# Performance work log

Measured on AMD Instinct MI355X. Metric: run time of the kernel, lower is better.

Reference implementation:

```python
import jax, jax.numpy as jnp
import numpy as np

N_NODES = 100000


def _gcn_conv(x, row, col, W, b, num_nodes):
    """PyG GCNConv: symmetric normalization with self-loops, then linear.
    row/col already include self-loops. x: [N, d_in], W: [d_in, d_out]."""
    xw = x @ W  # [N, d_out]
    ones = jnp.ones(row.shape[0], dtype=x.dtype)
    deg = jax.ops.segment_sum(ones, col, num_segments=num_nodes)  # in-degree incl self-loop
    deg_inv_sqrt = jnp.where(deg > 0, jax.lax.rsqrt(jnp.maximum(deg, 1e-12)), 0.0)
    norm = deg_inv_sqrt[row] * deg_inv_sqrt[col]  # [E]
    msgs = xw[row] * norm[:, None]  # gather + scale, [E, d_out]
    out = jax.ops.segment_sum(msgs, col, num_segments=num_nodes)  # scatter-add
    return out + b


def _add_self_loops(edge_index, num_nodes):
    loop = jnp.arange(num_nodes, dtype=edge_index.dtype)
    row = jnp.concatenate([edge_index[0], loop])
    col = jnp.concatenate([edge_index[1], loop])
    return row, col


def setup_inputs() -> dict:
    key = jax.random.key(0)
    k_x, k_e, k_w1, k_b1, k_w2, k_b2 = jax.random.split(key, 6)
    in_dim, hidden_dim, out_dim = 64, 64, 32
    n_edges = 1600000
    x = jax.random.normal(k_x, (N_NODES, in_dim), dtype=jnp.float32)
    edge_index = jax.random.randint(k_e, (2, n_edges), 0, N_NODES, dtype=jnp.int64)
    # Glorot init like PyG's GCNConv linear weights
    s1 = float(np.sqrt(6.0 / (in_dim + hidden_dim)))
    s2 = float(np.sqrt(6.0 / (hidden_dim + out_dim)))
    W1 = jax.random.uniform(k_w1, (in_dim, hidden_dim), minval=-s1, maxval=s1, dtype=jnp.float32)
    b1 = jnp.zeros((hidden_dim,), dtype=jnp.float32)
    W2 = jax.random.uniform(k_w2, (hidden_dim, out_dim), minval=-s2, maxval=s2, dtype=jnp.float32)
    b2 = jnp.zeros((out_dim,), dtype=jnp.float32)
    return {"x": x, "edge_index": edge_index, "W1": W1, "b1": b1, "W2": W2, "b2": b2}


def reference(x, edge_index, W1, b1, W2, b2):
    row, col = _add_self_loops(edge_index, N_NODES)
    h = jax.nn.relu(_gcn_conv(x, row, col, W1, b1, N_NODES))
    out = _gcn_conv(h, row, col, W2, b2, N_NODES)
    return out
```

## Files before the change

kernel.cpp:

```cpp
#include <hip/hip_runtime.h>

#define NN 100000
#define FB_SH 10
#define FB_N  1024
#define NFB   98
#define NBLK  256
#define BH_TOT (NFB * NBLK)

static __device__ __forceinline__ unsigned short f2bf(float f) {
    unsigned u = __float_as_uint(f);
    u += 0x7fffu + ((u >> 16) & 1u);
    return (unsigned short)(u >> 16);
}
static __device__ __forceinline__ float bf2f(unsigned short h) {
    return __uint_as_float(((unsigned)h) << 16);
}


__global__ __launch_bounds__(256) void k_hist1(const int* __restrict__ coli,
                                               int* __restrict__ bhist, int E, int chunk) {
    __shared__ int h[NFB];
    for (int i = threadIdx.x; i < NFB; i += 256) h[i] = 0;
    __syncthreads();
    int bk = blockIdx.x;
    int beg = bk * chunk, end = min(E, beg + chunk);
    for (int e = beg + threadIdx.x; e < end; e += 256)
        atomicAdd(&h[coli[e] >> FB_SH], 1);
    __syncthreads();
    for (int i = threadIdx.x; i < NFB; i += 256)
        bhist[i * NBLK + bk] = h[i];
}

__global__ __launch_bounds__(1024) void k_scanA(int* __restrict__ a,
                                                int* __restrict__ blksum, int n) {
    __shared__ int sh[1024];
    int i = blockIdx.x * 1024 + threadIdx.x;
    int v = (i < n) ? a[i] : 0;
    sh[threadIdx.x] = v;
    __syncthreads();
    #pragma unroll
    for (int d = 1; d < 1024; d <<= 1) {
        int t = (threadIdx.x >= d) ? sh[threadIdx.x - d] : 0;
        __syncthreads();
        sh[threadIdx.x] += t;
        __syncthreads();
    }
    if (i < n) a[i] = sh[threadIdx.x] - v;
    if (threadIdx.x == 1023) blksum[blockIdx.x] = sh[1023];
}

__global__ void k_scanB(int* __restrict__ blksum, int nb, int* __restrict__ off, int E) {
    if (threadIdx.x == 0 && blockIdx.x == 0) {
        int s = 0;
        for (int b = 0; b < nb; ++b) { int t = blksum[b]; blksum[b] = s; s += t; }
        off[NN] = E;
    }
}

__global__ __launch_bounds__(256) void k_scanC(int* __restrict__ a,
                                               const int* __restrict__ blksum, int n) {
    int i = blockIdx.x * 256 + threadIdx.x;
    if (i < n) a[i] += blksum[i >> 10];
}

__global__ __launch_bounds__(256) void k_bin2(
    const int* __restrict__ rowi, const int* __restrict__ coli,
    const int* __restrict__ bbase, unsigned int* __restrict__ cbin, int E, int chunk)
{
    __shared__ int cur[NFB];
    int bk = blockIdx.x;
    for (int i = threadIdx.x; i < NFB; i += 256) cur[i] = bbase[i * NBLK + bk];
    __syncthreads();
    int beg = bk * chunk, end = min(E, beg + chunk);
    for (int e = beg + threadIdx.x; e < end; e += 256) {
        int col = coli[e];
        int row = rowi[e];
        int b = col >> FB_SH;
        unsigned int val = ((unsigned int)row << FB_SH) | (unsigned int)(col & (FB_N - 1));
        int pos = atomicAdd(&cur[b], 1);
        cbin[pos] = val;
    }
}

__global__ __launch_bounds__(1024) void k_csr(
    const unsigned int* __restrict__ cbin, const int* __restrict__ bbase,
    int* __restrict__ off, float* __restrict__ dinv,
    int* __restrict__ srcs, int n, int E)
{
    __shared__ int hist[FB_N];
    __shared__ int wsum[16];
    int b = blockIdx.x;
    int beg = bbase[b * NBLK];
    int end = (b + 1 < NFB) ? bbase[(b + 1) * NBLK] : E;
    int tid = threadIdx.x;
    hist[tid] = 0;
    __syncthreads();
    for (int e = beg + tid; e < end; e += 1024)
        atomicAdd(&hist[cbin[e] & (FB_N - 1)], 1);
    __syncthreads();
    int v = hist[tid];
    int lane = tid & 63;
    int wid  = tid >> 6;
    int incl = v;
    #pragma unroll
    for (int d = 1; d < 64; d <<= 1) {
        int t = __shfl_up(incl, d, 64);
        if (lane >= d) incl += t;
    }
    if (lane == 63) wsum[wid] = incl;
    __syncthreads();
    if (wid == 0) {
        int ws = (lane < 16) ? wsum[lane] : 0;
        int wincl = ws;
        #pragma unroll
        for (int d = 1; d < 16; d <<= 1) {
            int t = __shfl_up(wincl, d, 64);
            if (lane >= d) wincl += t;
        }
        if (lane < 16) wsum[lane] = wincl - ws;
    }
    __syncthreads();
    int excl = wsum[wid] + incl - v;
    int node = (b << FB_SH) + tid;
    if (node < n) {
        off[node]  = beg + excl;
        dinv[node] = rsqrtf((float)(v + 1));
    }
    __syncthreads();
    hist[tid] = excl;
    __syncthreads();
    for (int e = beg + tid; e < end; e += 1024) {
        unsigned int pv = cbin[e];
        int cl  = (int)(pv & (FB_N - 1));
        int row = (int)(pv >> FB_SH);
        int p = atomicAdd(&hist[cl], 1);
        srcs[beg + p] = row;
    }
}

template<int DOUT>
__global__ __launch_bounds__(256) void k_gemm_scale(
    const float* __restrict__ X, const float* __restrict__ W,
    const float* __restrict__ dinv, unsigned short* __restrict__ Ybf, int n)
{
    constexpr int TPR = DOUT / 4;
    constexpr int R   = 256 / TPR;
    __shared__ float sW[64 * DOUT];
    __shared__ float sX[R * 64];

    for (int i = threadIdx.x; i < 64 * DOUT; i += 256) sW[i] = W[i];
    int r0 = blockIdx.x * R;
    for (int i = threadIdx.x; i < R * 64; i += 256) {
        int r = r0 + (i >> 6);
        sX[i] = (r < n) ? X[(size_t)r * 64 + (i & 63)] : 0.0f;
    }
    __syncthreads();

    int lr  = threadIdx.x / TPR;
    int c4  = (threadIdx.x % TPR) * 4;
    int row = r0 + lr;
    const float* xr = &sX[lr * 64];
    float4 acc = make_float4(0.f, 0.f, 0.f, 0.f);
    #pragma unroll
    for (int k = 0; k < 64; ++k) {
        float xv = xr[k];
        const float* wr = &sW[k * DOUT + c4];
        acc.x = fmaf(xv, wr[0], acc.x);
        acc.y = fmaf(xv, wr[1], acc.y);
        acc.z = fmaf(xv, wr[2], acc.z);
        acc.w = fmaf(xv, wr[3], acc.w);
    }
    if (row < n) {
        float s = dinv[row];
        ushort4 o;
        o.x = f2bf(acc.x * s);
        o.y = f2bf(acc.y * s);
        o.z = f2bf(acc.z * s);
        o.w = f2bf(acc.w * s);
        *(ushort4*)&Ybf[(size_t)row * DOUT + c4] = o;
    }
}

template<bool RELU>
__global__ __launch_bounds__(256) void k_agg64(
    const unsigned short* __restrict__ Ybf, const int* __restrict__ off,
    const int* __restrict__ srcs, const float* __restrict__ dinv,
    const float* __restrict__ bias, float* __restrict__ O, int n)
{
    int node = blockIdx.x * 4 + (threadIdx.x >> 6);
    if (node >= n) return;
    int c = threadIdx.x & 63;
    int j = off[node], end = off[node + 1];
    float s0 = bf2f(Ybf[(size_t)node * 64 + c]);
    float s1 = 0.f, s2 = 0.f, s3 = 0.f, s4 = 0.f, s5 = 0.f, s6 = 0.f, s7 = 0.f;
    for (; j + 8 <= end; j += 8) {
        int i0 = srcs[j],     i1 = srcs[j + 1], i2 = srcs[j + 2], i3 = srcs[j + 3];
        int i4 = srcs[j + 4], i5 = srcs[j + 5], i6 = srcs[j + 6], i7 = srcs[j + 7];
        unsigned short r0 = Ybf[(size_t)i0 * 64 + c];
        unsigned short r1 = Ybf[(size_t)i1 * 64 + c];
        unsigned short r2 = Ybf[(size_t)i2 * 64 + c];
        unsigned short r3 = Ybf[(size_t)i3 * 64 + c];
        unsigned short r4 = Ybf[(size_t)i4 * 64 + c];
        unsigned short r5 = Ybf[(size_t)i5 * 64 + c];
        unsigned short r6 = Ybf[(size_t)i6 * 64 + c];
        unsigned short r7 = Ybf[(size_t)i7 * 64 + c];
        s0 += bf2f(r0); s1 += bf2f(r1); s2 += bf2f(r2); s3 += bf2f(r3);
        s4 += bf2f(r4); s5 += bf2f(r5); s6 += bf2f(r6); s7 += bf2f(r7);
    }
    for (; j < end; ++j) s0 += bf2f(Ybf[(size_t)srcs[j] * 64 + c]);
    float s = ((s0 + s1) + (s2 + s3)) + ((s4 + s5) + (s6 + s7));
    float o = fmaf(dinv[node], s, bias[c]);
    if (RELU) o = fmaxf(o, 0.f);
    O[(size_t)node * 64 + c] = o;
}

template<bool RELU>
__global__ __launch_bounds__(256) void k_agg32(
    const unsigned short* __restrict__ Ybf, const int* __restrict__ off,
    const int* __restrict__ srcs, const float* __restrict__ dinv,
    const float* __restrict__ bias, float* __restrict__ O, int n)
{
    int node = blockIdx.x * 8 + (threadIdx.x >> 5);
    if (node >= n) return;
    int c = threadIdx.x & 31;
    int j = off[node], end = off[node + 1];
    float s0 = bf2f(Ybf[(size_t)node * 32 + c]);
    float s1 = 0.f, s2 = 0.f, s3 = 0.f, s4 = 0.f, s5 = 0.f, s6 = 0.f, s7 = 0.f;
    for (; j + 8 <= end; j += 8) {
        int i0 = srcs[j],     i1 = srcs[j + 1], i2 = srcs[j + 2], i3 = srcs[j + 3];
        int i4 = srcs[j + 4], i5 = srcs[j + 5], i6 = srcs[j + 6], i7 = srcs[j + 7];
        unsigned short r0 = Ybf[(size_t)i0 * 32 + c];
        unsigned short r1 = Ybf[(size_t)i1 * 32 + c];
        unsigned short r2 = Ybf[(size_t)i2 * 32 + c];
        unsigned short r3 = Ybf[(size_t)i3 * 32 + c];
        unsigned short r4 = Ybf[(size_t)i4 * 32 + c];
        unsigned short r5 = Ybf[(size_t)i5 * 32 + c];
        unsigned short r6 = Ybf[(size_t)i6 * 32 + c];
        unsigned short r7 = Ybf[(size_t)i7 * 32 + c];
        s0 += bf2f(r0); s1 += bf2f(r1); s2 += bf2f(r2); s3 += bf2f(r3);
        s4 += bf2f(r4); s5 += bf2f(r5); s6 += bf2f(r6); s7 += bf2f(r7);
    }
    for (; j < end; ++j) s0 += bf2f(Ybf[(size_t)srcs[j] * 32 + c]);
    float s = ((s0 + s1) + (s2 + s3)) + ((s4 + s5) + (s6 + s7));
    float o = fmaf(dinv[node], s, bias[c]);
    if (RELU) o = fmaxf(o, 0.f);
    O[(size_t)node * 32 + c] = o;
}

extern "C" void kernel_launch(void* const* d_in, const int* in_sizes, int n_in,
                              void* d_out, int out_size, void* d_ws, size_t ws_size,
                              hipStream_t stream) {
    const float* x  = (const float*)d_in[0];
    const int*   ei = (const int*)d_in[1];
    const float* W1 = (const float*)d_in[2];
    const float* b1 = (const float*)d_in[3];
    const float* W2 = (const float*)d_in[4];
    const float* b2 = (const float*)d_in[5];
    float* out = (float*)d_out;

    const int n = NN;
    const int E = in_sizes[1] / 2;
    const int* rowi = ei;
    const int* coli = ei + E;
    const int chunk = (E + NBLK - 1) / NBLK;

    char* p = (char*)d_ws;
    auto alloc = [&p](size_t bytes) { char* q = p; p += (bytes + 255) & ~(size_t)255; return q; };
    int*   bhist  = (int*)alloc((size_t)BH_TOT * 4);
    int*   blksum = (int*)alloc(32 * 4);
    int*   off    = (int*)alloc((size_t)(n + 1) * 4);
    float* dinv   = (float*)alloc((size_t)n * 4);
    int*   srcs   = (int*)alloc((size_t)E * 4);
    unsigned short* Ybf1 = (unsigned short*)alloc((size_t)n * 64 * 2);
    unsigned short* Ybf2 = (unsigned short*)alloc((size_t)n * 32 * 2);
    float* H      = (float*)alloc((size_t)n * 64 * 4);
    unsigned int* cbin = (unsigned int*)H;

    k_hist1<<<NBLK, 256, 0, stream>>>(coli, bhist, E, chunk);
    int nbs = (BH_TOT + 1023) / 1024;
    k_scanA<<<nbs, 1024, 0, stream>>>(bhist, blksum, BH_TOT);
    k_scanB<<<1, 64, 0, stream>>>(blksum, nbs, off, E);
    k_scanC<<<(BH_TOT + 255) / 256, 256, 0, stream>>>(bhist, blksum, BH_TOT);
    k_bin2<<<NBLK, 256, 0, stream>>>(rowi, coli, bhist, cbin, E, chunk);
    k_csr<<<NFB, 1024, 0, stream>>>(cbin, bhist, off, dinv, srcs, n, E);

    k_gemm_scale<64><<<(n + 15) / 16, 256, 0, stream>>>(x, W1, dinv, Ybf1, n);
    k_agg64<true><<<(n + 3) / 4, 256, 0, stream>>>(Ybf1, off, srcs, dinv, b1, H, n);

    k_gemm_scale<32><<<(n + 31) / 32, 256, 0, stream>>>(H, W2, dinv, Ybf2, n);
    k_agg32<false><<<(n + 7) / 8, 256, 0, stream>>>(Ybf2, off, srcs, dinv, b2, out, n);
}
```

Baseline: 205.0 us.

## Split neighbor edges across wavefront lanes with vectorized bf16 gathers in aggregation

Both aggregation kernels now give each wavefront lane two channels loaded as ushort2, so a 64-lane wavefront covers 2 (agg64) or 4 (agg32) neighbor rows at a time. Partial sums are combined with xor shuffles. agg32 moves from a 32-thread group per node to a full 64-lane wavefront per node, with the launch grid adjusted to match. The aim is wider gather loads and more neighbors in flight per instruction, at the cost of shuffle reductions and half or more of the lanes sitting idle during the final write.

```diff
diff --git a/kernel.cpp b/kernel.cpp
--- a/kernel.cpp
+++ b/kernel.cpp
@@ -189,29 +189,44 @@
 {
     int node = blockIdx.x * 4 + (threadIdx.x >> 6);
     if (node >= n) return;
-    int c = threadIdx.x & 63;
-    int j = off[node], end = off[node + 1];
-    float s0 = bf2f(Ybf[(size_t)node * 64 + c]);
-    float s1 = 0.f, s2 = 0.f, s3 = 0.f, s4 = 0.f, s5 = 0.f, s6 = 0.f, s7 = 0.f;
-    for (; j + 8 <= end; j += 8) {
-        int i0 = srcs[j],     i1 = srcs[j + 1], i2 = srcs[j + 2], i3 = srcs[j + 3];
-        int i4 = srcs[j + 4], i5 = srcs[j + 5], i6 = srcs[j + 6], i7 = srcs[j + 7];
-        unsigned short r0 = Ybf[(size_t)i0 * 64 + c];
-        unsigned short r1 = Ybf[(size_t)i1 * 64 + c];
-        unsigned short r2 = Ybf[(size_t)i2 * 64 + c];
-        unsigned short r3 = Ybf[(size_t)i3 * 64 + c];
-        unsigned short r4 = Ybf[(size_t)i4 * 64 + c];
-        unsigned short r5 = Ybf[(size_t)i5 * 64 + c];
-        unsigned short r6 = Ybf[(size_t)i6 * 64 + c];
-        unsigned short r7 = Ybf[(size_t)i7 * 64 + c];
-        s0 += bf2f(r0); s1 += bf2f(r1); s2 += bf2f(r2); s3 += bf2f(r3);
-        s4 += bf2f(r4); s5 += bf2f(r5); s6 += bf2f(r6); s7 += bf2f(r7);
-    }
-    for (; j < end; ++j) s0 += bf2f(Ybf[(size_t)srcs[j] * 64 + c]);
-    float s = ((s0 + s1) + (s2 + s3)) + ((s4 + s5) + (s6 + s7));
-    float o = fmaf(dinv[node], s, bias[c]);
-    if (RELU) o = fmaxf(o, 0.f);
-    O[(size_t)node * 64 + c] = o;
+    int l  = threadIdx.x & 63;
+    int h  = l >> 5;
+    int ch = (l & 31) * 2;
+    int beg = off[node], end = off[node + 1];
+    float a0 = 0.f, a1 = 0.f;
+    int j = beg;
+    for (; j + 16 <= end; j += 16) {
+        #pragma unroll
+        for (int k = 0; k < 8; ++k) {
+            int src = srcs[j + 2 * k + h];
+            ushort2 u = *(const ushort2*)&Ybf[(size_t)src * 64 + ch];
+            a0 += bf2f(u.x); a1 += bf2f(u.y);
+        }
+    }
+    for (; j + 2 <= end; j += 2) {
+        int src = srcs[j + h];
+        ushort2 u = *(const ushort2*)&Ybf[(size_t)src * 64 + ch];
+        a0 += bf2f(u.x); a1 += bf2f(u.y);
+    }
+    if (h == 0) {
+        if (j < end) {
+            int src = srcs[j];
+            ushort2 u = *(const ushort2*)&Ybf[(size_t)src * 64 + ch];
+            a0 += bf2f(u.x); a1 += bf2f(u.y);
+        }
+        ushort2 u = *(const ushort2*)&Ybf[(size_t)node * 64 + ch];
+        a0 += bf2f(u.x); a1 += bf2f(u.y);
+    }
+    a0 += __shfl_xor(a0, 32, 64);
+    a1 += __shfl_xor(a1, 32, 64);
+    if (h == 0) {
+        float d = dinv[node];
+        float2 o;
+        o.x = fmaf(d, a0, bias[ch]);
+        o.y = fmaf(d, a1, bias[ch + 1]);
+        if (RELU) { o.x = fmaxf(o.x, 0.f); o.y = fmaxf(o.y, 0.f); }
+        *(float2*)&O[(size_t)node * 64 + ch] = o;
+    }
 }
 
 template<bool RELU>
@@ -220,31 +235,48 @@
     const int* __restrict__ srcs, const float* __restrict__ dinv,
     const float* __restrict__ bias, float* __restrict__ O, int n)
 {
-    int node = blockIdx.x * 8 + (threadIdx.x >> 5);
+    int node = blockIdx.x * 4 + (threadIdx.x >> 6);
     if (node >= n) return;
-    int c = threadIdx.x & 31;
-    int j = off[node], end = off[node + 1];
-    float s0 = bf2f(Ybf[(size_t)node * 32 + c]);
-    float s1 = 0.f, s2 = 0.f, s3 = 0.f, s4 = 0.f, s5 = 0.f, s6 = 0.f, s7 = 0.f;
-    for (; j + 8 <= end; j += 8) {
-        int i0 = srcs[j],     i1 = srcs[j + 1], i2 = srcs[j + 2], i3 = srcs[j + 3];
-        int i4 = srcs[j + 4], i5 = srcs[j + 5], i6 = srcs[j + 6], i7 = srcs[j + 7];
-        unsigned short r0 = Ybf[(size_t)i0 * 32 + c];
-        unsigned short r1 = Ybf[(size_t)i1 * 32 + c];
-        unsigned short r2 = Ybf[(size_t)i2 * 32 + c];
-        unsigned short r3 = Ybf[(size_t)i3 * 32 + c];
-        unsigned short r4 = Ybf[(size_t)i4 * 32 + c];
-        unsigned short r5 = Ybf[(size_t)i5 * 32 + c];
-        unsigned short r6 = Ybf[(size_t)i6 * 32 + c];
-        unsigned short r7 = Ybf[(size_t)i7 * 32 + c];
-        s0 += bf2f(r0); s1 += bf2f(r1); s2 += bf2f(r2); s3 += bf2f(r3);
-        s4 += bf2f(r4); s5 += bf2f(r5); s6 += bf2f(r6); s7 += bf2f(r7);
-    }
-    for (; j < end; ++j) s0 += bf2f(Ybf[(size_t)srcs[j] * 32 + c]);
-    float s = ((s0 + s1) + (s2 + s3)) + ((s4 + s5) + (s6 + s7));
-    float o = fmaf(dinv[node], s, bias[c]);
-    if (RELU) o = fmaxf(o, 0.f);
-    O[(size_t)node * 32 + c] = o;
+    int l  = threadIdx.x & 63;
+    int q  = l >> 4;
+    int ch = (l & 15) * 2;
+    int beg = off[node], end = off[node + 1];
+    float a0 = 0.f, a1 = 0.f;
+    int j = beg;
+    for (; j + 16 <= end; j += 16) {
+        #pragma unroll
+        for (int k = 0; k < 4; ++k) {
+            int src = srcs[j + 4 * k + q];
+            ushort2 u = *(const ushort2*)&Ybf[(size_t)src * 32 + ch];
+            a0 += bf2f(u.x); a1 += bf2f(u.y);
+        }
+    }
+    for (; j + 4 <= end; j += 4) {
+        int src = srcs[j + q];
+        ushort2 u = *(const ushort2*)&Ybf[(size_t)src * 32 + ch];
+        a0 += bf2f(u.x); a1 += bf2f(u.y);
+    }
+    if (q < end - j) {
+        int src = srcs[j + q];
+        ushort2 u = *(const ushort2*)&Ybf[(size_t)src * 32 + ch];
+        a0 += bf2f(u.x); a1 += bf2f(u.y);
+    }
+    if (q == 0) {
+        ushort2 u = *(const ushort2*)&Ybf[(size_t)node * 32 + ch];
+        a0 += bf2f(u.x); a1 += bf2f(u.y);
+    }
+    a0 += __shfl_xor(a0, 16, 64);
+    a1 += __shfl_xor(a1, 16, 64);
+    a0 += __shfl_xor(a0, 32, 64);
+    a1 += __shfl_xor(a1, 32, 64);
+    if (q == 0) {
+        float d = dinv[node];
+        float2 o;
+        o.x = fmaf(d, a0, bias[ch]);
+        o.y = fmaf(d, a1, bias[ch + 1]);
+        if (RELU) { o.x = fmaxf(o.x, 0.f); o.y = fmaxf(o.y, 0.f); }
+        *(float2*)&O[(size_t)node * 32 + ch] = o;
+    }
 }
 
 extern "C" void kernel_launch(void* const* d_in, const int* in_sizes, int n_in,
@@ -288,5 +320,5 @@
     k_agg64<true><<<(n + 3) / 4, 256, 0, stream>>>(Ybf1, off, srcs, dinv, b1, H, n);
 
     k_gemm_scale<32><<<(n + 31) / 32, 256, 0, stream>>>(H, W2, dinv, Ybf2, n);
-    k_agg32<false><<<(n + 7) / 8, 256, 0, stream>>>(Ybf2, off, srcs, dinv, b2, out, n);
-}
+    k_agg32<false><<<(n + 3) / 4, 256, 0, stream>>>(Ybf2, off, srcs, dinv, b2, out, n);
+}
```

Result: slower. 209.7 us (+2.3%).
